# Optimization experiments

Hardware: AMD Instinct MI355X
Metric: run time of the kernel (lower is better)

Reference implementation:

```python
import jax, jax.numpy as jnp
import numpy as np

B, C, P, H, W = 64, 2048, 4, 14, 14
HID = C * P // 2  # 4096
S = H * W         # 196


def setup_inputs() -> dict:
    key = jax.random.key(0)
    k1, k2, k3, k4, k5 = jax.random.split(key, 5)
    x = jax.random.normal(k1, (B, C, H, W), dtype=jnp.float32)
    w1 = jax.random.normal(k2, (HID, C), dtype=jnp.float32) * 0.02
    b1 = jnp.zeros((HID,), dtype=jnp.float32)
    w2 = jax.random.normal(k3, (C * P, HID), dtype=jnp.float32) * 0.02
    b2 = jnp.zeros((C * P,), dtype=jnp.float32)
    return {"x": x, "w1": w1, "b1": b1, "w2": w2, "b2": b2}


def reference(x, w1, b1, w2, b2):
    # SE-style gating: global average pool -> fc1 -> sigmoid -> fc2 -> sigmoid
    g = x.mean(axis=(2, 3))                                  # [B, C]
    h = jax.nn.sigmoid(g @ w1.T + b1)                        # [B, HID]
    w = jax.nn.sigmoid(h @ w2.T + b2).reshape(B, P, C)       # grouping_result [B, P, C]
    # Weighted feature: mean over channels of w[b,p,c] * x[b,c,s].
    # Original materializes [B,P,C,196] then AdaptiveAvgPool3d over C;
    # mathematically this is a batched matmul divided by C.
    xs = x.reshape(B, C, S)                                  # [B, C, 196]
    feat = jnp.einsum('bpc,bcs->bps', w, xs) / C             # [B, P, 196]
    return (w, feat.reshape(B, P, H, W))
```

## Files before the change

kernel.cpp:

```cpp
#include <hip/hip_runtime.h>
#include <cstdint>
#include <cstddef>

typedef __attribute__((ext_vector_type(4))) float  f32x4;
typedef __attribute__((ext_vector_type(8))) short  short8;

__device__ __forceinline__ short f2bf(float f) {
  unsigned u = __float_as_uint(f);
  u += 0x7FFF + ((u >> 16) & 1);
  return (short)(u >> 16);
}
__device__ __forceinline__ float sigmoidf(float x) {
  return 1.0f / (1.0f + __expf(-x));
}

__global__ __launch_bounds__(256) void pool_kernel(const float* __restrict__ x,
                                                   short* __restrict__ g,
                                                   int nrows) {
  int gid  = blockIdx.x * 256 + threadIdx.x;
  int row  = gid >> 6;
  int lane = threadIdx.x & 63;
  if (row >= nrows) return;
  float s = 0.f;
  if (lane < 49) {
    const float4* p = (const float4*)(x + (size_t)row * 196);
    float4 v = p[lane];
    s = v.x + v.y + v.z + v.w;
  }
#pragma unroll
  for (int off = 32; off > 0; off >>= 1) s += __shfl_down(s, off);
  if (lane == 0) g[row] = f2bf(s * (1.0f / 196.0f));
}

template<int N, int K, bool OUT_BF16>
__global__ __launch_bounds__(512, 4) void gemm_fused(const short* __restrict__ A,
                                                     const float* __restrict__ B,
                                                     const float* __restrict__ bias,
                                                     void* __restrict__ outp) {
  constexpr int KW = K / 8;
  constexpr int NK = KW / 32;
  const int n0  = blockIdx.x * 16;
  const int tid = threadIdx.x;
  const int l   = tid & 63;
  const int wv  = tid >> 6;
  const int kw0 = wv * KW;

  __shared__ float red[8 * 1024];

  const int ko = (l >> 4) * 8;
  const float* Bp = B + (size_t)(n0 + (l & 15)) * K + kw0 + ko;
  const short* Ap = A + (size_t)(l & 15) * K + kw0 + ko;

  f32x4 acc0 = {}, acc1 = {}, acc2 = {}, acc3 = {};

  f32x4 bc0 = __builtin_nontemporal_load((const f32x4*)Bp);
  f32x4 bc1 = __builtin_nontemporal_load((const f32x4*)(Bp + 4));
  short8 ac0 = *(const short8*)(Ap);
  short8 ac1 = *(const short8*)(Ap + 16 * K);
  short8 ac2 = *(const short8*)(Ap + 32 * K);
  short8 ac3 = *(const short8*)(Ap + 48 * K);

  for (int t = 0; t < NK; ++t) {
    f32x4 bn0 = {}, bn1 = {};
    short8 an0 = {}, an1 = {}, an2 = {}, an3 = {};
    if (t + 1 < NK) {
      const float* bp = Bp + (t + 1) * 32;
      const short* ap = Ap + (t + 1) * 32;
      bn0 = __builtin_nontemporal_load((const f32x4*)bp);
      bn1 = __builtin_nontemporal_load((const f32x4*)(bp + 4));
      an0 = *(const short8*)(ap);
      an1 = *(const short8*)(ap + 16 * K);
      an2 = *(const short8*)(ap + 32 * K);
      an3 = *(const short8*)(ap + 48 * K);
    }
    short8 bb;
    bb[0] = f2bf(bc0[0]); bb[1] = f2bf(bc0[1]); bb[2] = f2bf(bc0[2]); bb[3] = f2bf(bc0[3]);
    bb[4] = f2bf(bc1[0]); bb[5] = f2bf(bc1[1]); bb[6] = f2bf(bc1[2]); bb[7] = f2bf(bc1[3]);
    acc0 = __builtin_amdgcn_mfma_f32_16x16x32_bf16(ac0, bb, acc0, 0, 0, 0);
    acc1 = __builtin_amdgcn_mfma_f32_16x16x32_bf16(ac1, bb, acc1, 0, 0, 0);
    acc2 = __builtin_amdgcn_mfma_f32_16x16x32_bf16(ac2, bb, acc2, 0, 0, 0);
    acc3 = __builtin_amdgcn_mfma_f32_16x16x32_bf16(ac3, bb, acc3, 0, 0, 0);
    bc0 = bn0; bc1 = bn1;
    ac0 = an0; ac1 = an1; ac2 = an2; ac3 = an3;
  }

  {
    float* rw = red + wv * 1024;
    const int mb = (l >> 4) << 2;
    const int nn = l & 15;
#pragma unroll
    for (int r = 0; r < 4; ++r) rw[(0  + mb + r) * 16 + nn] = acc0[r];
#pragma unroll
    for (int r = 0; r < 4; ++r) rw[(16 + mb + r) * 16 + nn] = acc1[r];
#pragma unroll
    for (int r = 0; r < 4; ++r) rw[(32 + mb + r) * 16 + nn] = acc2[r];
#pragma unroll
    for (int r = 0; r < 4; ++r) rw[(48 + mb + r) * 16 + nn] = acc3[r];
  }
  __syncthreads();

#pragma unroll
  for (int i = tid; i < 1024; i += 512) {
    float s = 0.f;
#pragma unroll
    for (int w = 0; w < 8; ++w) s += red[w * 1024 + i];
    int m  = i >> 4;
    int nn = n0 + (i & 15);
    s = sigmoidf(s + bias[nn]);
    if constexpr (OUT_BF16) ((short*)outp)[(size_t)m * N + nn] = f2bf(s);
    else                    ((float*)outp)[(size_t)m * N + nn] = s;
  }
}

__global__ __launch_bounds__(256) void einsum_part(const float* __restrict__ x,
                                                   const float* __restrict__ wg,
                                                   float* __restrict__ fpart) {
  const int b  = blockIdx.x >> 4;
  const int cc = blockIdx.x & 15;
  __shared__ float gs[4 * 128];
  const int tid = threadIdx.x;
  const float* wb = wg + (size_t)b * 8192 + cc * 128;
#pragma unroll
  for (int i = 0; i < 2; ++i) {
    int idx = i * 256 + tid;
    int p = idx >> 7, c = idx & 127;
    gs[idx] = wb[p * 2048 + c];
  }
  __syncthreads();
  if (tid < 196) {
    const float* xp = x + (size_t)b * 2048 * 196 + (size_t)cc * 128 * 196 + tid;
    float a0 = 0, a1 = 0, a2 = 0, a3 = 0;
#pragma unroll 8
    for (int c = 0; c < 128; ++c) {
      float xv = xp[(size_t)c * 196];
      a0 += gs[c]       * xv;
      a1 += gs[128 + c] * xv;
      a2 += gs[256 + c] * xv;
      a3 += gs[384 + c] * xv;
    }
    float* fp = fpart + ((size_t)(b * 16 + cc) * 4) * 196 + tid;
    fp[0]   = a0;
    fp[196] = a1;
    fp[392] = a2;
    fp[588] = a3;
  }
}

__global__ __launch_bounds__(256) void feat_reduce(const float* __restrict__ fpart,
                                                   float* __restrict__ feat) {
  int i = blockIdx.x * 256 + threadIdx.x;
  if (i >= 64 * 4 * 196) return;
  int s = i % 196;
  int p = (i / 196) & 3;
  int b = i / 784;
  float sum = 0.f;
#pragma unroll
  for (int cc = 0; cc < 16; ++cc)
    sum += fpart[((size_t)(b * 16 + cc) * 4 + p) * 196 + s];
  feat[i] = sum * (1.0f / 2048.0f);
}

extern "C" void kernel_launch(void* const* d_in, const int* in_sizes, int n_in,
                              void* d_out, int out_size, void* d_ws, size_t ws_size,
                              hipStream_t stream) {
  const float* x  = (const float*)d_in[0];
  const float* w1 = (const float*)d_in[1];
  const float* b1 = (const float*)d_in[2];
  const float* w2 = (const float*)d_in[3];
  const float* b2 = (const float*)d_in[4];
  float* out = (float*)d_out;

  short* g_bf  = (short*)d_ws;
  short* h_bf  = g_bf + 64 * 2048;
  float* fpart = (float*)((char*)d_ws + (1 << 20));

  float* wout = out;
  float* feat = out + 524288;

  pool_kernel<<<(64 * 2048) / 4, 256, 0, stream>>>(x, g_bf, 64 * 2048);

  gemm_fused<4096, 2048, true><<<4096 / 16, 512, 0, stream>>>(g_bf, w1, b1, h_bf);

  gemm_fused<8192, 4096, false><<<8192 / 16, 512, 0, stream>>>(h_bf, w2, b2, wout);

  einsum_part<<<64 * 16, 256, 0, stream>>>(x, wout, fpart);

  feat_reduce<<<(50176 + 255) / 256, 256, 0, stream>>>(fpart, feat);
}
```

Measured before the change: 112.3 us.

## Replace feat partial-sum reduction kernel with atomics; zero feat inside fc2 GEMM

Drops the separate feat_reduce launch and the fpart workspace. The einsum kernel now atomically adds its scaled per-chunk partial sums straight into the output, and the fc2 GEMM zeroes the feat buffer (512 blocks × 98 floats) so no extra memset launch is needed. The einsum also reads the gating weights directly from global memory instead of staging them in LDS, and the GEMM switches weight loads from nontemporal to regular loads. The cost is atomic contention (16 adds per output element) and a non-deterministic summation order.

```diff
diff --git a/kernel.cpp b/kernel.cpp
--- a/kernel.cpp
+++ b/kernel.cpp
@@ -32,11 +32,12 @@
   if (lane == 0) g[row] = f2bf(s * (1.0f / 196.0f));
 }
 
-template<int N, int K, bool OUT_BF16>
+template<int N, int K, bool OUT_BF16, bool ZERO_FEAT>
 __global__ __launch_bounds__(512, 4) void gemm_fused(const short* __restrict__ A,
                                                      const float* __restrict__ B,
                                                      const float* __restrict__ bias,
-                                                     void* __restrict__ outp) {
+                                                     void* __restrict__ outp,
+                                                     float* __restrict__ zbuf) {
   constexpr int KW = K / 8;
   constexpr int NK = KW / 32;
   const int n0  = blockIdx.x * 16;
@@ -44,6 +45,10 @@
   const int l   = tid & 63;
   const int wv  = tid >> 6;
   const int kw0 = wv * KW;
+
+  if constexpr (ZERO_FEAT) {
+    if (tid < 98) zbuf[blockIdx.x * 98 + tid] = 0.f;
+  }
 
   __shared__ float red[8 * 1024];
 
@@ -53,8 +58,8 @@
 
   f32x4 acc0 = {}, acc1 = {}, acc2 = {}, acc3 = {};
 
-  f32x4 bc0 = __builtin_nontemporal_load((const f32x4*)Bp);
-  f32x4 bc1 = __builtin_nontemporal_load((const f32x4*)(Bp + 4));
+  f32x4 bc0 = *(const f32x4*)(Bp);
+  f32x4 bc1 = *(const f32x4*)(Bp + 4);
   short8 ac0 = *(const short8*)(Ap);
   short8 ac1 = *(const short8*)(Ap + 16 * K);
   short8 ac2 = *(const short8*)(Ap + 32 * K);
@@ -66,8 +71,8 @@
     if (t + 1 < NK) {
       const float* bp = Bp + (t + 1) * 32;
       const short* ap = Ap + (t + 1) * 32;
-      bn0 = __builtin_nontemporal_load((const f32x4*)bp);
-      bn1 = __builtin_nontemporal_load((const f32x4*)(bp + 4));
+      bn0 = *(const f32x4*)(bp);
+      bn1 = *(const f32x4*)(bp + 4);
       an0 = *(const short8*)(ap);
       an1 = *(const short8*)(ap + 16 * K);
       an2 = *(const short8*)(ap + 32 * K);
@@ -112,52 +117,29 @@
   }
 }
 
-__global__ __launch_bounds__(256) void einsum_part(const float* __restrict__ x,
-                                                   const float* __restrict__ wg,
-                                                   float* __restrict__ fpart) {
-  const int b  = blockIdx.x >> 4;
-  const int cc = blockIdx.x & 15;
-  __shared__ float gs[4 * 128];
+__global__ __launch_bounds__(256) void einsum_kernel(const float* __restrict__ x,
+                                                     const float* __restrict__ wg,
+                                                     float* __restrict__ feat) {
+  const int b   = blockIdx.x >> 4;
+  const int cc  = blockIdx.x & 15;
   const int tid = threadIdx.x;
-  const float* wb = wg + (size_t)b * 8192 + cc * 128;
-#pragma unroll
-  for (int i = 0; i < 2; ++i) {
-    int idx = i * 256 + tid;
-    int p = idx >> 7, c = idx & 127;
-    gs[idx] = wb[p * 2048 + c];
+  if (tid >= 196) return;
+  const float* wp = wg + (size_t)b * 8192 + cc * 128;
+  const float* xp = x + (size_t)b * 2048 * 196 + (size_t)cc * 128 * 196 + tid;
+  float a0 = 0.f, a1 = 0.f, a2 = 0.f, a3 = 0.f;
+#pragma unroll 8
+  for (int c = 0; c < 128; ++c) {
+    float xv = xp[(size_t)c * 196];
+    a0 = __builtin_fmaf(wp[c],        xv, a0);
+    a1 = __builtin_fmaf(wp[2048 + c], xv, a1);
+    a2 = __builtin_fmaf(wp[4096 + c], xv, a2);
+    a3 = __builtin_fmaf(wp[6144 + c], xv, a3);
   }
-  __syncthreads();
-  if (tid < 196) {
-    const float* xp = x + (size_t)b * 2048 * 196 + (size_t)cc * 128 * 196 + tid;
-    float a0 = 0, a1 = 0, a2 = 0, a3 = 0;
-#pragma unroll 8
-    for (int c = 0; c < 128; ++c) {
-      float xv = xp[(size_t)c * 196];
-      a0 += gs[c]       * xv;
-      a1 += gs[128 + c] * xv;
-      a2 += gs[256 + c] * xv;
-      a3 += gs[384 + c] * xv;
-    }
-    float* fp = fpart + ((size_t)(b * 16 + cc) * 4) * 196 + tid;
-    fp[0]   = a0;
-    fp[196] = a1;
-    fp[392] = a2;
-    fp[588] = a3;
-  }
-}
-
-__global__ __launch_bounds__(256) void feat_reduce(const float* __restrict__ fpart,
-                                                   float* __restrict__ feat) {
-  int i = blockIdx.x * 256 + threadIdx.x;
-  if (i >= 64 * 4 * 196) return;
-  int s = i % 196;
-  int p = (i / 196) & 3;
-  int b = i / 784;
-  float sum = 0.f;
-#pragma unroll
-  for (int cc = 0; cc < 16; ++cc)
-    sum += fpart[((size_t)(b * 16 + cc) * 4 + p) * 196 + s];
-  feat[i] = sum * (1.0f / 2048.0f);
+  const float invC = 1.0f / 2048.0f;
+  atomicAdd(feat + (b * 4 + 0) * 196 + tid, a0 * invC);
+  atomicAdd(feat + (b * 4 + 1) * 196 + tid, a1 * invC);
+  atomicAdd(feat + (b * 4 + 2) * 196 + tid, a2 * invC);
+  atomicAdd(feat + (b * 4 + 3) * 196 + tid, a3 * invC);
 }
 
 extern "C" void kernel_launch(void* const* d_in, const int* in_sizes, int n_in,
@@ -170,20 +152,17 @@
   const float* b2 = (const float*)d_in[4];
   float* out = (float*)d_out;
 
-  short* g_bf  = (short*)d_ws;
-  short* h_bf  = g_bf + 64 * 2048;
-  float* fpart = (float*)((char*)d_ws + (1 << 20));
+  short* g_bf = (short*)d_ws;
+  short* h_bf = g_bf + 64 * 2048;
 
   float* wout = out;
   float* feat = out + 524288;
 
   pool_kernel<<<(64 * 2048) / 4, 256, 0, stream>>>(x, g_bf, 64 * 2048);
 
-  gemm_fused<4096, 2048, true><<<4096 / 16, 512, 0, stream>>>(g_bf, w1, b1, h_bf);
+  gemm_fused<4096, 2048, true, false><<<4096 / 16, 512, 0, stream>>>(g_bf, w1, b1, h_bf, nullptr);
 
-  gemm_fused<8192, 4096, false><<<8192 / 16, 512, 0, stream>>>(h_bf, w2, b2, wout);
+  gemm_fused<8192, 4096, false, true><<<8192 / 16, 512, 0, stream>>>(h_bf, w2, b2, wout, feat);
 
-  einsum_part<<<64 * 16, 256, 0, stream>>>(x, wout, fpart);
-
-  feat_reduce<<<(50176 + 255) / 256, 256, 0, stream>>>(fpart, feat);
+  einsum_kernel<<<64 * 16, 256, 0, stream>>>(x, wout, feat);
 }
```

Result: faster. 103.8 us (-7.6%).
